# Performance work log

Measured on AMD Instinct MI355X. Metric: run time of the kernel, lower is better.

The kernel has to match this reference:

```python
import jax, jax.numpy as jnp
import numpy as np

D_MODEL = 1024
NUM_HEADS = 16
HEAD_DIM = D_MODEL // NUM_HEADS


def setup_inputs() -> dict:
    key = jax.random.key(0)
    ks = jax.random.split(key, 9)
    s = 1.0 / np.sqrt(D_MODEL)
    return {
        "x": jax.random.normal(ks[0], (4, 2048, D_MODEL), dtype=jnp.float32),
        "Wq": jax.random.uniform(ks[1], (D_MODEL, D_MODEL), minval=-s, maxval=s, dtype=jnp.float32),
        "bq": jax.random.uniform(ks[2], (D_MODEL,), minval=-s, maxval=s, dtype=jnp.float32),
        "Wk": jax.random.uniform(ks[3], (D_MODEL, D_MODEL), minval=-s, maxval=s, dtype=jnp.float32),
        "bk": jax.random.uniform(ks[4], (D_MODEL,), minval=-s, maxval=s, dtype=jnp.float32),
        "Wv": jax.random.uniform(ks[5], (D_MODEL, D_MODEL), minval=-s, maxval=s, dtype=jnp.float32),
        "bv": jax.random.uniform(ks[6], (D_MODEL,), minval=-s, maxval=s, dtype=jnp.float32),
        "Wo": jax.random.uniform(ks[7], (D_MODEL, D_MODEL), minval=-s, maxval=s, dtype=jnp.float32),
        "bo": jax.random.uniform(ks[8], (D_MODEL,), minval=-s, maxval=s, dtype=jnp.float32),
    }


def reference(x, Wq, bq, Wk, bk, Wv, bv, Wo, bo):
    B, T, C = x.shape
    H, Dh = NUM_HEADS, HEAD_DIM
    # projections (nn.Linear applies x @ W^T + b)
    q = (x @ Wq.T + bq).reshape(B, T, H, Dh).transpose(0, 2, 1, 3)  # [B,H,T,Dh]
    k = (x @ Wk.T + bk).reshape(B, T, H, Dh).transpose(0, 2, 1, 3)
    v = (x @ Wv.T + bv).reshape(B, T, H, Dh).transpose(0, 2, 1, 3)
    scale = 1.0 / np.sqrt(Dh).astype(np.float32)
    att = jnp.einsum("bhqd,bhkd->bhqk", q, k) * scale  # [B,H,T,T]
    causal = jnp.tril(jnp.ones((T, T), dtype=bool))
    att = jnp.where(causal[None, None], att, -jnp.inf)
    att = jax.nn.softmax(att, axis=-1)
    # dropout is identity in eval mode
    out = jnp.einsum("bhqk,bhkd->bhqd", att, v)  # [B,H,T,Dh]
    out = out.transpose(0, 2, 1, 3).reshape(B, T, C)
    return out @ Wo.T + bo
```

## Files before the change

### kernel.cpp

```cpp
#include <hip/hip_runtime.h>
#include <stdint.h>

typedef __attribute__((ext_vector_type(8))) short short8;
typedef __attribute__((ext_vector_type(4))) short short4v;
typedef __attribute__((ext_vector_type(4))) float floatx4;

#define QSCALE 0.1803368801111f

__device__ __forceinline__ unsigned short f2bf(float f) {
  unsigned int u = __float_as_uint(f);
  unsigned int r = (u + 0x7FFFu + ((u >> 16) & 1u)) >> 16;
  return (unsigned short)r;
}

__device__ __forceinline__ unsigned int cvt_pk_bf16(float lo, float hi) {
  unsigned int r;
  asm("v_cvt_pk_bf16_f32 %0, %1, %2" : "=v"(r) : "v"(lo), "v"(hi));
  return r;
}

__device__ __forceinline__ void async_copy16(void* lds, const void* g) {
  __builtin_amdgcn_global_load_lds(
      (const __attribute__((address_space(1))) unsigned int*)g,
      (__attribute__((address_space(3))) unsigned int*)lds, 16, 0, 0);
}

__global__ __launch_bounds__(256) void f2ball_kernel(
    const float* __restrict__ x, unsigned short* __restrict__ xb,
    const float* __restrict__ w0, const float* __restrict__ w1,
    const float* __restrict__ w2, const float* __restrict__ w3,
    unsigned short* __restrict__ o0, unsigned short* __restrict__ o1,
    unsigned short* __restrict__ o2, unsigned short* __restrict__ o3) {
  const float* in;
  unsigned short* out;
  long i;
  if (blockIdx.x < 8192) {
    in = x;
    out = xb;
    i = (long)blockIdx.x * 256 + threadIdx.x;
  } else {
    int wb = blockIdx.x - 8192;
    int which = wb >> 10;
    in = (which == 0) ? w0 : (which == 1) ? w1 : (which == 2) ? w2 : w3;
    out = (which == 0) ? o0 : (which == 1) ? o1 : (which == 2) ? o2 : o3;
    i = (long)(wb & 1023) * 256 + threadIdx.x;
  }
  float4 v = ((const float4*)in)[i];
  short4v o;
  o[0] = (short)f2bf(v.x);
  o[1] = (short)f2bf(v.y);
  o[2] = (short)f2bf(v.z);
  o[3] = (short)f2bf(v.w);
  *(short4v*)(out + i * 4) = o;
}

__device__ __forceinline__ void gemm128_mainloop_db(
    const unsigned short* __restrict__ A, const unsigned short* __restrict__ Bt,
    int K, long brow, long bcol, unsigned short* As, unsigned short* Bs,
    floatx4 acc[4][4]) {
  const int tid = threadIdx.x;
  const int wave = tid >> 6;
  const int lane = tid & 63;
  const int wr = wave >> 1, wc = wave & 1;
  const int lr = lane & 15, lg = lane >> 4;

  const unsigned short* ga = A + (brow + (tid >> 2)) * (long)K + (tid & 3) * 8;
  const unsigned short* gb = Bt + (bcol + (tid >> 2)) * (long)K + (tid & 3) * 8;
  const int woff = wave * 512;
  const int a_off = (wr * 64 + lr) * 32 + lg * 8;
  const int b_off = (wc * 64 + lr) * 32 + lg * 8;

  async_copy16(As + woff, ga);
  async_copy16(As + woff + 2048, ga + (long)64 * K);
  async_copy16(Bs + woff, gb);
  async_copy16(Bs + woff + 2048, gb + (long)64 * K);
  ga += 32;
  gb += 32;
  __syncthreads();

  int buf = 0;
  for (int kt = 0; kt < K; kt += 32) {
    if (kt + 32 < K) {
      unsigned short* lA = As + (buf ^ 1) * 4096 + woff;
      unsigned short* lB = Bs + (buf ^ 1) * 4096 + woff;
      async_copy16(lA, ga);
      async_copy16(lA + 2048, ga + (long)64 * K);
      async_copy16(lB, gb);
      async_copy16(lB + 2048, gb + (long)64 * K);
      ga += 32;
      gb += 32;
    }
    const unsigned short* Ab = As + buf * 4096;
    const unsigned short* Bb = Bs + buf * 4096;
    short8 af[4], bf[4];
#pragma unroll
    for (int i = 0; i < 4; ++i) {
      af[i] = *(const short8*)(Ab + a_off + i * 512);
      bf[i] = *(const short8*)(Bb + b_off + i * 512);
    }
#pragma unroll
    for (int i = 0; i < 4; ++i)
#pragma unroll
      for (int j = 0; j < 4; ++j)
        acc[i][j] = __builtin_amdgcn_mfma_f32_16x16x32_bf16(af[i], bf[j], acc[i][j], 0, 0, 0);
    __syncthreads();
    buf ^= 1;
  }
}

__global__ __launch_bounds__(256, 4) void qkv_gemm(
    const unsigned short* __restrict__ xb, const unsigned short* __restrict__ wqkv,
    const float* __restrict__ bq, const float* __restrict__ bk,
    const float* __restrict__ bv, unsigned short* __restrict__ q_out,
    unsigned short* __restrict__ k_out, unsigned short* __restrict__ vt_out) {
  __shared__ __align__(16) unsigned short Sh[128 * 136];
  unsigned short* As = Sh;
  unsigned short* Bs = Sh + 8192;
  floatx4 zero = {0.f, 0.f, 0.f, 0.f};
  floatx4 acc[4][4];
#pragma unroll
  for (int i = 0; i < 4; ++i)
#pragma unroll
    for (int j = 0; j < 4; ++j) acc[i][j] = zero;

  long brow = (long)blockIdx.x * 128;
  long bcol = (long)blockIdx.y * 128;
  gemm128_mainloop_db(xb, wqkv, 1024, brow, bcol, As, Bs, acc);

  const int wave = threadIdx.x >> 6, lane = threadIdx.x & 63;
  const int wr = wave >> 1, wc = wave & 1, lr = lane & 15, lg = lane >> 4;
  const int kind = (int)(bcol >> 10);
  const float* bias = (kind == 0) ? bq : (kind == 1 ? bk : bv);

  if (kind == 2) {
#pragma unroll
    for (int i = 0; i < 4; ++i)
#pragma unroll
      for (int j = 0; j < 4; ++j) {
        int n_local = wc * 64 + j * 16 + lr;
        int m_base = wr * 64 + i * 16 + lg * 4;
        float bsc = bias[(int)((bcol + n_local) & 1023)];
        short4v pk;
#pragma unroll
        for (int r = 0; r < 4; ++r) pk[r] = (short)f2bf(acc[i][j][r] + bsc);
        *(short4v*)(Sh + n_local * 136 + m_base) = pk;
      }
    __syncthreads();
    const int b = (int)(brow >> 11);
    const int t0 = (int)(brow & 2047);
    const int f0 = (int)(bcol - 2048);
#pragma unroll
    for (int p = 0; p < 8; ++p) {
      int c = p * 256 + threadIdx.x;
      int d_loc = c >> 4, tc = c & 15;
      short8 v = *(const short8*)(Sh + d_loc * 136 + tc * 8);
      int h = (f0 >> 6) + (d_loc >> 6);
      int d = d_loc & 63;
      *(short8*)(vt_out + ((long)((b * 16 + h) * 64 + d)) * 2048 + t0 + tc * 8) = v;
    }
  } else {
#pragma unroll
    for (int i = 0; i < 4; ++i)
#pragma unroll
      for (int j = 0; j < 4; ++j)
#pragma unroll
        for (int r = 0; r < 4; ++r) {
          int m = (int)brow + wr * 64 + i * 16 + lg * 4 + r;
          int n = (int)bcol + wc * 64 + j * 16 + lr;
          int f = n & 1023;
          float v = acc[i][j][r] + bias[f];
          if (kind == 0) v *= QSCALE;
          unsigned short o = f2bf(v);
          int h = f >> 6, d = f & 63;
          int bb = m >> 11, t = m & 2047;
          long bh = (long)(bb * 16 + h);
          if (kind == 0)
            q_out[(bh * 2048 + t) * 64 + d] = o;
          else
            k_out[(bh * 2048 + t) * 64 + d] = o;
        }
  }
}

__global__ __launch_bounds__(256, 4) void out_gemm(
    const unsigned short* __restrict__ ob, const unsigned short* __restrict__ wo,
    const float* __restrict__ bo, float* __restrict__ out) {
  __shared__ unsigned short As[2 * 128 * 32];
  __shared__ unsigned short Bs[2 * 128 * 32];
  floatx4 zero = {0.f, 0.f, 0.f, 0.f};
  floatx4 acc[4][4];
#pragma unroll
  for (int i = 0; i < 4; ++i)
#pragma unroll
    for (int j = 0; j < 4; ++j) acc[i][j] = zero;

  long brow = (long)blockIdx.x * 128;
  long bcol = (long)blockIdx.y * 128;
  gemm128_mainloop_db(ob, wo, 1024, brow, bcol, As, Bs, acc);

  const int wave = threadIdx.x >> 6, lane = threadIdx.x & 63;
  const int wr = wave >> 1, wc = wave & 1, lr = lane & 15, lg = lane >> 4;
#pragma unroll
  for (int i = 0; i < 4; ++i)
#pragma unroll
    for (int j = 0; j < 4; ++j)
#pragma unroll
      for (int r = 0; r < 4; ++r) {
        int m = (int)brow + wr * 64 + i * 16 + lg * 4 + r;
        int n = (int)bcol + wc * 64 + j * 16 + lr;
        out[(long)m * 1024 + n] = acc[i][j][r] + bo[n];
      }
}

__device__ __forceinline__ void stage_kv(char* __restrict__ Kb, char* __restrict__ Vb,
                                         const char* __restrict__ Kp,
                                         const char* __restrict__ Vt, int kv0,
                                         int tid) {
  const int wave = tid >> 6;
#pragma unroll
  for (int j = 0; j < 2; ++j) {
    int d = j * 256 + tid;
    int row = d >> 3, cc = d & 7;
    int gc = cc ^ (row & 7);
    const char* gk = Kp + (size_t)kv0 * 128 + row * 128 + gc * 16;
    async_copy16(Kb + (j * 256 + wave * 64) * 16, gk);
    const char* gv = Vt + (size_t)row * 4096 + (size_t)kv0 * 2 + gc * 16;
    async_copy16(Vb + (j * 256 + wave * 64) * 16, gv);
  }
}

__device__ __forceinline__ void qk_tile(floatx4 (&s)[2][4], const char* __restrict__ Kb,
                                        const short8 (&qf)[2][2], int lr, int lg) {
  floatx4 zero = {0.f, 0.f, 0.f, 0.f};
  const int x7 = lr & 7;
  __builtin_amdgcn_s_setprio(1);
#pragma unroll
  for (int nt = 0; nt < 4; ++nt) {
    const char* kr = Kb + (nt * 16 + lr) * 128;
    short8 kf0 = *(const short8*)(kr + ((lg ^ x7) * 16));
    short8 kf1 = *(const short8*)(kr + (((4 + lg) ^ x7) * 16));
#pragma unroll
    for (int qa = 0; qa < 2; ++qa) {
      floatx4 a = zero;
      a = __builtin_amdgcn_mfma_f32_16x16x32_bf16(kf0, qf[qa][0], a, 0, 0, 0);
      a = __builtin_amdgcn_mfma_f32_16x16x32_bf16(kf1, qf[qa][1], a, 0, 0, 0);
      s[qa][nt] = a;
    }
  }
  __builtin_amdgcn_s_setprio(0);
}

__device__ __forceinline__ void sm_pv(
    floatx4 (&s)[2][4], const char* __restrict__ Vb, char* __restrict__ PTw,
    int kv0, int q0, int lr, int lg, bool diag,
    float (&m_i)[2], float (&l_i)[2], floatx4 (&accO)[2][4]) {
  const int x7 = lr & 7;
  if (diag) {
#pragma unroll
    for (int qa = 0; qa < 2; ++qa) {
      const int q = q0 + qa * 16 + lr;
#pragma unroll
      for (int nt = 0; nt < 4; ++nt)
#pragma unroll
        for (int r = 0; r < 4; ++r) {
          int kvi = kv0 + nt * 16 + lg * 4 + r;
          if (kvi > q) s[qa][nt][r] = -1e30f;
        }
    }
  }

  float pmax[2];
#pragma unroll
  for (int qa = 0; qa < 2; ++qa) {
    float m0 = fmaxf(fmaxf(s[qa][0][0], s[qa][0][1]), fmaxf(s[qa][0][2], s[qa][0][3]));
    float m1 = fmaxf(fmaxf(s[qa][1][0], s[qa][1][1]), fmaxf(s[qa][1][2], s[qa][1][3]));
    float m2 = fmaxf(fmaxf(s[qa][2][0], s[qa][2][1]), fmaxf(s[qa][2][2], s[qa][2][3]));
    float m3 = fmaxf(fmaxf(s[qa][3][0], s[qa][3][1]), fmaxf(s[qa][3][2], s[qa][3][3]));
    pmax[qa] = fmaxf(fmaxf(m0, m1), fmaxf(m2, m3));
  }

  float g = fmaxf(pmax[0] - m_i[0], pmax[1] - m_i[1]);
  if (__any(g > 11.5f)) {
#pragma unroll
    for (int qa = 0; qa < 2; ++qa) {
      float mx = fmaxf(pmax[qa], __shfl_xor(pmax[qa], 16));
      mx = fmaxf(mx, __shfl_xor(mx, 32));
      float mnew = fmaxf(m_i[qa], mx);
      float scl = exp2f(m_i[qa] - mnew);
      m_i[qa] = mnew;
      l_i[qa] *= scl;
#pragma unroll
      for (int r = 0; r < 4; ++r) {
        float so = __shfl(scl, lg * 4 + r);
#pragma unroll
        for (int dt = 0; dt < 4; ++dt) accO[qa][dt][r] *= so;
      }
    }
  }

#pragma unroll
  for (int qa = 0; qa < 2; ++qa) {
    char* prow = PTw + (qa * 16 + lr) * 128;
#pragma unroll
    for (int nt = 0; nt < 4; ++nt) {
      float p0 = exp2f(s[qa][nt][0] - m_i[qa]);
      float p1 = exp2f(s[qa][nt][1] - m_i[qa]);
      float p2 = exp2f(s[qa][nt][2] - m_i[qa]);
      float p3 = exp2f(s[qa][nt][3] - m_i[qa]);
      l_i[qa] += (p0 + p1) + (p2 + p3);
      uint2 wv;
      wv.x = cvt_pk_bf16(p0, p1);
      wv.y = cvt_pk_bf16(p2, p3);
      *(uint2*)(prow + (((2 * nt + (lg >> 1)) ^ x7) * 16) + ((2 * lg) & 3) * 4) = wv;
    }
  }

  __builtin_amdgcn_s_setprio(1);
#pragma unroll
  for (int kk = 0; kk < 2; ++kk) {
    short8 pf0 = *(const short8*)(PTw + lr * 128 + (((4 * kk + lg) ^ x7) * 16));
    short8 pf1 = *(const short8*)(PTw + (16 + lr) * 128 + (((4 * kk + lg) ^ x7) * 16));
#pragma unroll
    for (int dt = 0; dt < 4; ++dt) {
      short8 vf = *(const short8*)(Vb + (dt * 16 + lr) * 128 + (((4 * kk + lg) ^ x7) * 16));
      accO[0][dt] = __builtin_amdgcn_mfma_f32_16x16x32_bf16(pf0, vf, accO[0][dt], 0, 0, 0);
      accO[1][dt] = __builtin_amdgcn_mfma_f32_16x16x32_bf16(pf1, vf, accO[1][dt], 0, 0, 0);
    }
  }
  __builtin_amdgcn_s_setprio(0);
}

__global__ __launch_bounds__(256, 2) void attn_fwd(
    const unsigned short* __restrict__ qb, const unsigned short* __restrict__ kb,
    const unsigned short* __restrict__ vtb, unsigned short* __restrict__ ob) {
  __shared__ __align__(16) char Kbuf[3][8192];
  __shared__ __align__(16) char Vbuf[3][8192];
  __shared__ __align__(16) char PTbuf[4][4096];

  const int bh = blockIdx.x * 8 + (blockIdx.y & 7);
  const int pr = blockIdx.y >> 3;

  const int tid = threadIdx.x;
  const int wave = tid >> 6, lane = tid & 63;
  const int lr = lane & 15, lg = lane >> 4;
  const unsigned short* Q = qb + (long)bh * 2048 * 64;
  const char* Kp = (const char*)(kb + (long)bh * 2048 * 64);
  const char* Vt = (const char*)(vtb + (long)bh * 64 * 2048);
  const int b = bh >> 4, h = bh & 15;
  char* PTw = PTbuf[wave];

  floatx4 zero = {0.f, 0.f, 0.f, 0.f};

#pragma unroll 1
  for (int half = 0; half < 2; ++half) {
    const int qt = half ? (15 - pr) : pr;
    const int q0 = qt * 128 + wave * 32;
    const int nkv = 2 * qt + 2;

    short8 qf[2][2];
#pragma unroll
    for (int qa = 0; qa < 2; ++qa)
#pragma unroll
      for (int kk = 0; kk < 2; ++kk)
        qf[qa][kk] = *(const short8*)(Q + (q0 + qa * 16 + lr) * 64 + kk * 32 + lg * 8);

    floatx4 accO[2][4];
#pragma unroll
    for (int qa = 0; qa < 2; ++qa)
#pragma unroll
      for (int dt = 0; dt < 4; ++dt) accO[qa][dt] = zero;
    float m_i[2] = {-1e30f, -1e30f};
    float l_i[2] = {0.f, 0.f};

    stage_kv(Kbuf[0], Vbuf[0], Kp, Vt, 0, tid);
    __syncthreads();
    stage_kv(Kbuf[1], Vbuf[1], Kp, Vt, 64, tid);
    floatx4 sA[2][4], sB[2][4];
    qk_tile(sA, Kbuf[0], qf, lr, lg);

#pragma unroll 1
    for (int kv = 0; kv < nkv; kv += 2) {
      __syncthreads();
      if (kv + 2 < nkv)
        stage_kv(Kbuf[(kv + 2) % 3], Vbuf[(kv + 2) % 3], Kp, Vt, (kv + 2) * 64, tid);
      qk_tile(sB, Kbuf[(kv + 1) % 3], qf, lr, lg);
      sm_pv(sA, Vbuf[kv % 3], PTw, kv * 64, q0, lr, lg, kv >= 2 * qt, m_i, l_i, accO);
      __syncthreads();
      if (kv + 3 < nkv)
        stage_kv(Kbuf[(kv + 3) % 3], Vbuf[(kv + 3) % 3], Kp, Vt, (kv + 3) * 64, tid);
      if (kv + 2 < nkv) qk_tile(sA, Kbuf[(kv + 2) % 3], qf, lr, lg);
      sm_pv(sB, Vbuf[(kv + 1) % 3], PTw, (kv + 1) * 64, q0, lr, lg, kv + 1 >= 2 * qt,
            m_i, l_i, accO);
    }

#pragma unroll
    for (int qa = 0; qa < 2; ++qa) {
      float lt = l_i[qa] + __shfl_xor(l_i[qa], 16);
      lt += __shfl_xor(lt, 32);
      float linv = 1.f / lt;
#pragma unroll
      for (int r = 0; r < 4; ++r) {
        float io = __shfl(linv, lg * 4 + r);
        int tq = q0 + qa * 16 + 4 * lg + r;
#pragma unroll
        for (int dt = 0; dt < 4; ++dt)
          ob[((long)b * 2048 + tq) * 1024 + h * 64 + dt * 16 + lr] =
              f2bf(accO[qa][dt][r] * io);
      }
    }
  }
}

extern "C" void kernel_launch(void* const* d_in, const int* in_sizes, int n_in,
                              void* d_out, int out_size, void* d_ws, size_t ws_size,
                              hipStream_t stream) {
  const float* x = (const float*)d_in[0];
  const float* bq = (const float*)d_in[2];
  const float* bk = (const float*)d_in[4];
  const float* bv = (const float*)d_in[6];
  const float* bo = (const float*)d_in[8];
  float* out = (float*)d_out;

  char* ws = (char*)d_ws;
  unsigned short* xb = (unsigned short*)(ws);
  unsigned short* wqkv = (unsigned short*)(ws + (16l << 20));
  unsigned short* wob = (unsigned short*)(ws + (22l << 20));
  unsigned short* qb = (unsigned short*)(ws + (24l << 20));
  unsigned short* kb = (unsigned short*)(ws + (40l << 20));
  unsigned short* vtb = (unsigned short*)(ws + (56l << 20));
  unsigned short* ob = (unsigned short*)(ws + (72l << 20));

  f2ball_kernel<<<12288, 256, 0, stream>>>(
      x, xb, (const float*)d_in[1], (const float*)d_in[3], (const float*)d_in[5],
      (const float*)d_in[7], wqkv, wqkv + (1l << 20), wqkv + (2l << 20), wob);

  qkv_gemm<<<dim3(64, 24), 256, 0, stream>>>(xb, wqkv, bq, bk, bv, qb, kb, vtb);
  attn_fwd<<<dim3(8, 64), 256, 0, stream>>>(qb, kb, vtb, ob);
  out_gemm<<<dim3(64, 8), 256, 0, stream>>>(ob, wob, bo, out);
}
```

Before: 171.9 us.

## Simplify attention to double-buffered single-tile blocks with higher occupancy

The attention kernel drops the three-stage K/V ring and the software-pipelined QK/softmax split. It now uses a plain double buffer with one fused step per KV tile. Each block handles one query tile instead of a paired light/heavy tile, launching 1024 blocks ordered heaviest-first, and launch bounds rise to three blocks per CU. This cuts LDS use and register pressure so more waves can hide latency, but it gives up the explicit overlap of QK MFMAs with softmax and pays a barrier per tile.

```diff
diff --git a/kernel.cpp b/kernel.cpp
--- a/kernel.cpp
+++ b/kernel.cpp
@@ -229,10 +229,14 @@
   }
 }
 
-__device__ __forceinline__ void qk_tile(floatx4 (&s)[2][4], const char* __restrict__ Kb,
-                                        const short8 (&qf)[2][2], int lr, int lg) {
+__device__ __forceinline__ void attn_step(
+    const char* __restrict__ Kb, const char* __restrict__ Vb,
+    char* __restrict__ PTw, const short8 (&qf)[2][2],
+    int kv0, int q0, int lr, int lg, bool diag,
+    float (&m_i)[2], float (&l_i)[2], floatx4 (&accO)[2][4]) {
   floatx4 zero = {0.f, 0.f, 0.f, 0.f};
   const int x7 = lr & 7;
+  floatx4 s[2][4];
   __builtin_amdgcn_s_setprio(1);
 #pragma unroll
   for (int nt = 0; nt < 4; ++nt) {
@@ -248,13 +252,7 @@
     }
   }
   __builtin_amdgcn_s_setprio(0);
-}
-
-__device__ __forceinline__ void sm_pv(
-    floatx4 (&s)[2][4], const char* __restrict__ Vb, char* __restrict__ PTw,
-    int kv0, int q0, int lr, int lg, bool diag,
-    float (&m_i)[2], float (&l_i)[2], floatx4 (&accO)[2][4]) {
-  const int x7 = lr & 7;
+
   if (diag) {
 #pragma unroll
     for (int qa = 0; qa < 2; ++qa) {
@@ -330,15 +328,16 @@
   __builtin_amdgcn_s_setprio(0);
 }
 
-__global__ __launch_bounds__(256, 2) void attn_fwd(
+__global__ __launch_bounds__(256, 3) void attn_fwd(
     const unsigned short* __restrict__ qb, const unsigned short* __restrict__ kb,
     const unsigned short* __restrict__ vtb, unsigned short* __restrict__ ob) {
-  __shared__ __align__(16) char Kbuf[3][8192];
-  __shared__ __align__(16) char Vbuf[3][8192];
+  __shared__ __align__(16) char Kbuf[2][8192];
+  __shared__ __align__(16) char Vbuf[2][8192];
   __shared__ __align__(16) char PTbuf[4][4096];
 
-  const int bh = blockIdx.x * 8 + (blockIdx.y & 7);
-  const int pr = blockIdx.y >> 3;
+  const int id = blockIdx.x;
+  const int qt = 15 - (id >> 6);
+  const int bh = id & 63;
 
   const int tid = threadIdx.x;
   const int wave = tid >> 6, lane = tid & 63;
@@ -351,62 +350,48 @@
 
   floatx4 zero = {0.f, 0.f, 0.f, 0.f};
 
+  const int q0 = qt * 128 + wave * 32;
+  const int nkv = 2 * qt + 2;
+
+  short8 qf[2][2];
+#pragma unroll
+  for (int qa = 0; qa < 2; ++qa)
+#pragma unroll
+    for (int kk = 0; kk < 2; ++kk)
+      qf[qa][kk] = *(const short8*)(Q + (q0 + qa * 16 + lr) * 64 + kk * 32 + lg * 8);
+
+  floatx4 accO[2][4];
+#pragma unroll
+  for (int qa = 0; qa < 2; ++qa)
+#pragma unroll
+    for (int dt = 0; dt < 4; ++dt) accO[qa][dt] = zero;
+  float m_i[2] = {-1e30f, -1e30f};
+  float l_i[2] = {0.f, 0.f};
+
+  stage_kv(Kbuf[0], Vbuf[0], Kp, Vt, 0, tid);
+  __syncthreads();
 #pragma unroll 1
-  for (int half = 0; half < 2; ++half) {
-    const int qt = half ? (15 - pr) : pr;
-    const int q0 = qt * 128 + wave * 32;
-    const int nkv = 2 * qt + 2;
-
-    short8 qf[2][2];
-#pragma unroll
-    for (int qa = 0; qa < 2; ++qa)
-#pragma unroll
-      for (int kk = 0; kk < 2; ++kk)
-        qf[qa][kk] = *(const short8*)(Q + (q0 + qa * 16 + lr) * 64 + kk * 32 + lg * 8);
-
-    floatx4 accO[2][4];
-#pragma unroll
-    for (int qa = 0; qa < 2; ++qa)
-#pragma unroll
-      for (int dt = 0; dt < 4; ++dt) accO[qa][dt] = zero;
-    float m_i[2] = {-1e30f, -1e30f};
-    float l_i[2] = {0.f, 0.f};
-
-    stage_kv(Kbuf[0], Vbuf[0], Kp, Vt, 0, tid);
+  for (int kv = 0; kv < nkv; ++kv) {
+    if (kv + 1 < nkv)
+      stage_kv(Kbuf[(kv + 1) & 1], Vbuf[(kv + 1) & 1], Kp, Vt, (kv + 1) * 64, tid);
+    attn_step(Kbuf[kv & 1], Vbuf[kv & 1], PTw, qf, kv * 64, q0, lr, lg,
+              kv >= 2 * qt, m_i, l_i, accO);
     __syncthreads();
-    stage_kv(Kbuf[1], Vbuf[1], Kp, Vt, 64, tid);
-    floatx4 sA[2][4], sB[2][4];
-    qk_tile(sA, Kbuf[0], qf, lr, lg);
-
-#pragma unroll 1
-    for (int kv = 0; kv < nkv; kv += 2) {
-      __syncthreads();
-      if (kv + 2 < nkv)
-        stage_kv(Kbuf[(kv + 2) % 3], Vbuf[(kv + 2) % 3], Kp, Vt, (kv + 2) * 64, tid);
-      qk_tile(sB, Kbuf[(kv + 1) % 3], qf, lr, lg);
-      sm_pv(sA, Vbuf[kv % 3], PTw, kv * 64, q0, lr, lg, kv >= 2 * qt, m_i, l_i, accO);
-      __syncthreads();
-      if (kv + 3 < nkv)
-        stage_kv(Kbuf[(kv + 3) % 3], Vbuf[(kv + 3) % 3], Kp, Vt, (kv + 3) * 64, tid);
-      if (kv + 2 < nkv) qk_tile(sA, Kbuf[(kv + 2) % 3], qf, lr, lg);
-      sm_pv(sB, Vbuf[(kv + 1) % 3], PTw, (kv + 1) * 64, q0, lr, lg, kv + 1 >= 2 * qt,
-            m_i, l_i, accO);
-    }
-
-#pragma unroll
-    for (int qa = 0; qa < 2; ++qa) {
-      float lt = l_i[qa] + __shfl_xor(l_i[qa], 16);
-      lt += __shfl_xor(lt, 32);
-      float linv = 1.f / lt;
-#pragma unroll
-      for (int r = 0; r < 4; ++r) {
-        float io = __shfl(linv, lg * 4 + r);
-        int tq = q0 + qa * 16 + 4 * lg + r;
-#pragma unroll
-        for (int dt = 0; dt < 4; ++dt)
-          ob[((long)b * 2048 + tq) * 1024 + h * 64 + dt * 16 + lr] =
-              f2bf(accO[qa][dt][r] * io);
-      }
+  }
+
+#pragma unroll
+  for (int qa = 0; qa < 2; ++qa) {
+    float lt = l_i[qa] + __shfl_xor(l_i[qa], 16);
+    lt += __shfl_xor(lt, 32);
+    float linv = 1.f / lt;
+#pragma unroll
+    for (int r = 0; r < 4; ++r) {
+      float io = __shfl(linv, lg * 4 + r);
+      int tq = q0 + qa * 16 + 4 * lg + r;
+#pragma unroll
+      for (int dt = 0; dt < 4; ++dt)
+        ob[((long)b * 2048 + tq) * 1024 + h * 64 + dt * 16 + lr] =
+            f2bf(accO[qa][dt][r] * io);
     }
   }
 }
@@ -435,6 +420,6 @@
       (const float*)d_in[7], wqkv, wqkv + (1l << 20), wqkv + (2l << 20), wob);
 
   qkv_gemm<<<dim3(64, 24), 256, 0, stream>>>(xb, wqkv, bq, bk, bv, qb, kb, vtb);
-  attn_fwd<<<dim3(8, 64), 256, 0, stream>>>(qb, kb, vtb, ob);
+  attn_fwd<<<1024, 256, 0, stream>>>(qb, kb, vtb, ob);
   out_gemm<<<dim3(64, 8), 256, 0, stream>>>(ob, wob, bo, out);
 }
```

New measurement: 164.1 us. -4.5%, faster.
